# Performance work log

Hardware: AMD Instinct MI355X
Metric: run time of the kernel (lower is better)

Reference implementation:

```python
import jax, jax.numpy as jnp
import numpy as np

HID = 2048
HEADS = 16
HEAD = HID // HEADS  # 128
INTER = 8192
EPS = 1e-5
THETA = 10000.0
B, S = 2, 2048


def _layernorm(x, scale, bias):
    mu = jnp.mean(x, axis=-1, keepdims=True)
    var = jnp.var(x, axis=-1, keepdims=True)
    return (x - mu) * jax.lax.rsqrt(var + EPS) * scale + bias


def _rope(x, cos, sin):
    # x: [b,s,h,d]; adjacent pairs form complex numbers (per apply_rotary_emb)
    xr = x.reshape(*x.shape[:-1], HEAD // 2, 2)
    x0, x1 = xr[..., 0], xr[..., 1]
    o0 = x0 * cos - x1 * sin
    o1 = x0 * sin + x1 * cos
    return jnp.stack((o0, o1), axis=-1).reshape(x.shape)


def setup_inputs() -> dict:
    key = jax.random.key(0)
    ks = jax.random.split(key, 6)
    sc = 0.02
    return {
        "hidden_states": jax.random.normal(ks[0], (B, S, HID), jnp.float32),
        "attention_mask": jnp.zeros((B, 1, 1, S), jnp.float32),
        "w_qkv": (jax.random.normal(ks[1], (HID, 3 * HID), jnp.float32) * sc),
        "b_qkv": jnp.zeros((3 * HID,), jnp.float32),
        "w_o": (jax.random.normal(ks[2], (HID, HID), jnp.float32) * sc),
        "b_o": jnp.zeros((HID,), jnp.float32),
        "ln1_scale": jnp.ones((HID,), jnp.float32),
        "ln1_bias": jnp.zeros((HID,), jnp.float32),
        "ln2_scale": jnp.ones((HID,), jnp.float32),
        "ln2_bias": jnp.zeros((HID,), jnp.float32),
        "w_in": (jax.random.normal(ks[3], (HID, INTER), jnp.float32) * sc),
        "b_in": jnp.zeros((INTER,), jnp.float32),
        "w_out": (jax.random.normal(ks[4], (INTER, HID), jnp.float32) * sc),
        "b_out": jnp.zeros((HID,), jnp.float32),
    }


def reference(hidden_states, attention_mask, w_qkv, b_qkv, w_o, b_o,
              ln1_scale, ln1_bias, ln2_scale, ln2_bias,
              w_in, b_in, w_out, b_out):
    b, s, d = hidden_states.shape
    # ---- attention branch ----
    x1 = _layernorm(hidden_states, ln1_scale, ln1_bias)
    qkv = x1 @ w_qkv + b_qkv
    q, k, v = jnp.split(qkv, 3, axis=-1)
    q = q.reshape(b, s, HEADS, HEAD)
    k = k.reshape(b, s, HEADS, HEAD)
    v = v.reshape(b, s, HEADS, HEAD)
    # rotary embedding (complex pairing of adjacent elements)
    inv_freq = 1.0 / (THETA ** (jnp.arange(0, HEAD, 2, dtype=jnp.float32) / HEAD))
    freqs = jnp.arange(s, dtype=jnp.float32)[:, None] * inv_freq[None, :]  # [s, HEAD/2]
    cos = jnp.cos(freqs)[None, :, None, :]
    sin = jnp.sin(freqs)[None, :, None, :]
    q = _rope(q, cos, sin)
    k = _rope(k, cos, sin)
    # NOTE: source multiplies by sqrt(head_size) (faithful to original code)
    factor = jnp.sqrt(jnp.float32(HEAD))
    attn = jnp.einsum('bqhd,bkhd->bhqk', q, k) * factor  # [b,h,s,s]
    causal = jnp.tril(jnp.ones((s, s), dtype=bool))
    bias = jnp.where(causal, 0.0, jnp.finfo(jnp.float32).min)
    attn = attn + bias[None, None, :, :] + attention_mask
    p = jax.nn.softmax(attn, axis=-1)
    ao = jnp.einsum('bhqk,bkhd->bqhd', p, v).reshape(b, s, d)
    attn_out = ao @ w_o + b_o
    # ---- mlp branch (parallel residual) ----
    x2 = _layernorm(hidden_states, ln2_scale, ln2_bias)
    mlp = jax.nn.gelu(x2 @ w_in + b_in, approximate=False) @ w_out + b_out
    return mlp + hidden_states + attn_out
```

## Files before the change

### kernel.cpp

```cpp
#include <hip/hip_runtime.h>
#include <math.h>

#define HID 2048
#define NH 16
#define HD 128
#define INTER 8192
#define BB 2
#define SS 2048
#define MT (BB*SS)

typedef __bf16 bf16x8 __attribute__((ext_vector_type(8)));
typedef _Float16 f16x8 __attribute__((ext_vector_type(8)));
typedef float f32x4 __attribute__((ext_vector_type(4)));
typedef float f32x16 __attribute__((ext_vector_type(16)));
typedef unsigned short u16x8 __attribute__((ext_vector_type(8)));

__device__ __forceinline__ float bf2f(unsigned short u) {
  unsigned v = ((unsigned)u) << 16;
  return __builtin_bit_cast(float, v);
}
__device__ __forceinline__ unsigned short f2bf(float x) {
  unsigned u = __builtin_bit_cast(unsigned, x);
  u += 0x7fffu + ((u >> 16) & 1u);
  return (unsigned short)(u >> 16);
}
__device__ __forceinline__ unsigned short f2h(float x) {
  _Float16 h = (_Float16)x;
  return __builtin_bit_cast(unsigned short, h);
}
__device__ __forceinline__ void gll16(const void* g, const void* lds) {
  __builtin_amdgcn_global_load_lds(
      (const __attribute__((address_space(1))) void*)g,
      (__attribute__((address_space(3))) void*)lds, 16, 0, 0);
}
__device__ __forceinline__ int swz(int row) {
  return (row & 7) ^ ((row >> 2) & 4);
}

__global__ __launch_bounds__(256) void ln2k(
    const float* __restrict__ X, const float* __restrict__ s1,
    const float* __restrict__ b1, const float* __restrict__ s2,
    const float* __restrict__ b2, unsigned short* __restrict__ X1f,
    unsigned short* __restrict__ X2) {
  const int row = blockIdx.x;
  const int tid = threadIdx.x;
  const float* x = X + (long)row * HID;
  float4 v0 = ((const float4*)x)[tid * 2];
  float4 v1 = ((const float4*)x)[tid * 2 + 1];
  float s = v0.x + v0.y + v0.z + v0.w + v1.x + v1.y + v1.z + v1.w;
  float q = v0.x * v0.x + v0.y * v0.y + v0.z * v0.z + v0.w * v0.w +
            v1.x * v1.x + v1.y * v1.y + v1.z * v1.z + v1.w * v1.w;
#pragma unroll
  for (int off = 1; off < 64; off <<= 1) {
    s += __shfl_xor(s, off);
    q += __shfl_xor(q, off);
  }
  __shared__ float rs[4], rq[4];
  const int wid = tid >> 6, lane = tid & 63;
  if (lane == 0) { rs[wid] = s; rq[wid] = q; }
  __syncthreads();
  s = rs[0] + rs[1] + rs[2] + rs[3];
  q = rq[0] + rq[1] + rq[2] + rq[3];
  const float mu = s * (1.f / HID);
  const float var = q * (1.f / HID) - mu * mu;
  const float rstd = rsqrtf(var + 1e-5f);
  float xv[8] = {v0.x, v0.y, v0.z, v0.w, v1.x, v1.y, v1.z, v1.w};
  u16x8 o1, o2;
#pragma unroll
  for (int e = 0; e < 8; e++) {
    const int j = tid * 8 + e;
    const float xn = (xv[e] - mu) * rstd;
    o1[e] = f2h(xn * s1[j] + b1[j]);
    o2[e] = f2bf(xn * s2[j] + b2[j]);
  }
  *(u16x8*)(X1f + (long)row * HID + tid * 8) = o1;
  *(u16x8*)(X2 + (long)row * HID + tid * 8) = o2;
}

template <bool F16>
__global__ __launch_bounds__(256) void wtrans(const float* __restrict__ W,
                                              unsigned short* __restrict__ WT,
                                              int K, int N, int ldn, int coff) {
  (void)N;
  __shared__ float t[32][33];
  const int n0 = blockIdx.x * 32, k0 = blockIdx.y * 32;
  const int tx = threadIdx.x, ty = threadIdx.y;
#pragma unroll
  for (int r = 0; r < 4; r++)
    t[ty + r * 8][tx] = W[(long)(k0 + ty + r * 8) * ldn + coff + n0 + tx];
  __syncthreads();
#pragma unroll
  for (int r = 0; r < 4; r++) {
    const float v = t[tx][ty + r * 8];
    WT[(long)(n0 + ty + r * 8) * K + k0 + tx] = F16 ? f2h(v) : f2bf(v);
  }
}

__global__ void rope_tab(float2* __restrict__ rope) {
  const int s = blockIdx.x, i = threadIdx.x;
  const double ang = (double)s * pow(10000.0, -(double)i / 64.0);
  rope[s * 64 + i] = make_float2((float)cos(ang), (float)sin(ang));
}

__global__ __launch_bounds__(256) void gemmqkv(
    const unsigned short* __restrict__ A, const unsigned short* __restrict__ Bt,
    const float* __restrict__ bias, const float2* __restrict__ rope,
    unsigned short* __restrict__ QF, unsigned short* __restrict__ KF,
    unsigned short* __restrict__ Vb) {
  __shared__ unsigned short As[128 * 64];
  __shared__ unsigned short Bs[128 * 64];
  const int K = HID;
  const int tid = threadIdx.x;
  const int wid = tid >> 6, lane = tid & 63;
  const int l31 = lane & 31, lg = lane >> 5;
  const int wr = wid >> 1, wc = wid & 1;
  const long rA0 = (long)blockIdx.y * 128;
  const long rB0 = (long)blockIdx.x * 128;

  f32x16 acc[2][2] = {};

  for (int kt = 0; kt < K; kt += 64) {
#pragma unroll
    for (int i = 0; i < 4; i++) {
      const int lin = i * 4096 + wid * 1024 + (lane << 4);
      const int row = lin >> 7;
      const int cs = ((lin >> 4) & 7) ^ swz(row);
      gll16(A + (rA0 + row) * (long)K + kt + cs * 8,
            (const char*)As + (i * 4096 + wid * 1024));
      gll16(Bt + (rB0 + row) * (long)K + kt + cs * 8,
            (const char*)Bs + (i * 4096 + wid * 1024));
    }
    __syncthreads();
#pragma unroll
    for (int kk = 0; kk < 4; kk++) {
      f16x8 av[2], bv[2];
#pragma unroll
      for (int t = 0; t < 2; t++) {
        const int rowA = wr * 64 + t * 32 + l31;
        const int cha = (kk * 2 + lg) ^ swz(rowA);
        av[t] = *(const f16x8*)((const char*)As + rowA * 128 + cha * 16);
        const int rowB = wc * 64 + t * 32 + l31;
        const int chb = (kk * 2 + lg) ^ swz(rowB);
        bv[t] = *(const f16x8*)((const char*)Bs + rowB * 128 + chb * 16);
      }
#pragma unroll
      for (int mt = 0; mt < 2; mt++)
#pragma unroll
        for (int nt = 0; nt < 2; nt++)
          acc[mt][nt] = __builtin_amdgcn_mfma_f32_32x32x16_f16(
              av[mt], bv[nt], acc[mt][nt], 0, 0, 0);
    }
    __syncthreads();
  }

  const int b_ = (int)(rA0 >> 11);
#pragma unroll
  for (int mt = 0; mt < 2; mt++) {
#pragma unroll
    for (int nt = 0; nt < 2; nt++) {
      const int col = (int)rB0 + wc * 64 + nt * 32 + l31;
      const float bsv = bias[col];
      const int cq = col & 2047;
      const int i = (cq & 127) >> 1;
      const int hh = (cq >> 7) & 15;
      const int d = cq & 127;
#pragma unroll
      for (int reg = 0; reg < 16; reg++) {
        const int row = (int)rA0 + wr * 64 + mt * 32 + (reg & 3) +
                        8 * (reg >> 2) + 4 * lg;
        const int srow = row & 2047;
        const float v = acc[mt][nt][reg] + bsv;
        if (col < 4096) {
          const float p = __shfl_xor(v, 1);
          const float2 cs = rope[srow * 64 + i];
          const float o = ((lane & 1) == 0) ? (v * cs.x - p * cs.y)
                                            : (p * cs.y + v * cs.x);
          unsigned short* dst = (col < 2048) ? QF : KF;
          dst[((long)(b_ * NH + hh) * SS + srow) * HD + d] = f2h(o);
        } else {
          Vb[(long)row * HID + (col - 4096)] = f2bf(v);
        }
      }
    }
  }
}

__global__ __launch_bounds__(256) void vtrans(
    const unsigned short* __restrict__ Vb, unsigned short* __restrict__ VTb) {
  __shared__ unsigned short t[32][33];
  const int bh = blockIdx.z, b = bh >> 4, h = bh & 15;
  const int d0 = blockIdx.x * 32, s0 = blockIdx.y * 32;
  const int tx = threadIdx.x, ty = threadIdx.y;
#pragma unroll
  for (int r = 0; r < 4; r++) {
    const int s = s0 + ty + r * 8;
    t[ty + r * 8][tx] = Vb[((long)(b * SS + s)) * HID + h * HD + d0 + tx];
  }
  __syncthreads();
#pragma unroll
  for (int r = 0; r < 4; r++) {
    const int d = d0 + ty + r * 8;
    VTb[((long)bh * HD + d) * SS + s0 + tx] = t[tx][ty + r * 8];
  }
}

template <int MODE>
__global__ __launch_bounds__(256) void gemm128(
    const unsigned short* __restrict__ A, const unsigned short* __restrict__ Bt,
    const float* __restrict__ bias, void* __restrict__ Cout, int M, int N,
    int K, const float* __restrict__ residF,
    const unsigned short* __restrict__ residB) {
  (void)M;
  __shared__ unsigned short As[128 * 64];
  __shared__ unsigned short Bs[128 * 64];
  const int tid = threadIdx.x;
  const int wid = tid >> 6, lane = tid & 63;
  const int l31 = lane & 31, lg = lane >> 5;
  const int wr = wid >> 1, wc = wid & 1;
  const long rA0 = (long)blockIdx.y * 128;
  const long rB0 = (long)blockIdx.x * 128;

  f32x16 acc[2][2] = {};

  for (int kt = 0; kt < K; kt += 64) {
#pragma unroll
    for (int i = 0; i < 4; i++) {
      const int lin = i * 4096 + wid * 1024 + (lane << 4);
      const int row = lin >> 7;
      const int cs = ((lin >> 4) & 7) ^ swz(row);
      gll16(A + (rA0 + row) * (long)K + kt + cs * 8,
            (const char*)As + (i * 4096 + wid * 1024));
      gll16(Bt + (rB0 + row) * (long)K + kt + cs * 8,
            (const char*)Bs + (i * 4096 + wid * 1024));
    }
    __syncthreads();
#pragma unroll
    for (int kk = 0; kk < 4; kk++) {
      bf16x8 av[2], bv[2];
#pragma unroll
      for (int t = 0; t < 2; t++) {
        const int rowA = wr * 64 + t * 32 + l31;
        const int cha = (kk * 2 + lg) ^ swz(rowA);
        av[t] = *(const bf16x8*)((const char*)As + rowA * 128 + cha * 16);
        const int rowB = wc * 64 + t * 32 + l31;
        const int chb = (kk * 2 + lg) ^ swz(rowB);
        bv[t] = *(const bf16x8*)((const char*)Bs + rowB * 128 + chb * 16);
      }
#pragma unroll
      for (int mt = 0; mt < 2; mt++)
#pragma unroll
        for (int nt = 0; nt < 2; nt++)
          acc[mt][nt] = __builtin_amdgcn_mfma_f32_32x32x16_bf16(
              av[mt], bv[nt], acc[mt][nt], 0, 0, 0);
    }
    __syncthreads();
  }

#pragma unroll
  for (int mt = 0; mt < 2; mt++) {
#pragma unroll
    for (int nt = 0; nt < 2; nt++) {
      const long col = rB0 + wc * 64 + nt * 32 + l31;
      const float bsv = bias[col];
#pragma unroll
      for (int reg = 0; reg < 16; reg++) {
        const long row = rA0 + wr * 64 + mt * 32 + (reg & 3) +
                         8 * (reg >> 2) + 4 * lg;
        float v = acc[mt][nt][reg] + bsv;
        if (MODE == 1) v = 0.5f * v * (1.f + erff(v * 0.7071067811865475f));
        if (MODE == 2) {
          v += residF[row * N + col] + bf2f(residB[row * N + col]);
          ((float*)Cout)[row * N + col] = v;
        } else {
          ((unsigned short*)Cout)[row * N + col] = f2bf(v);
        }
      }
    }
  }
}

__global__ __launch_bounds__(512, 2) void flash(
    const unsigned short* __restrict__ QF, const unsigned short* __restrict__ KF,
    const unsigned short* __restrict__ VT, const float* __restrict__ amask,
    unsigned short* __restrict__ AO) {
  __shared__ unsigned short Kt[2][64 * 128];
  __shared__ unsigned short Vt[2][128 * 64];
  __shared__ unsigned short Pl[8 * 1024];
  __shared__ float maskL[SS];
  const int z = blockIdx.x;
  const int qt = 15 - (z >> 5);
  const int bh = z & 31;
  const int b = bh >> 4, h = bh & 15;
  const int tid = threadIdx.x, wid = tid >> 6, lane = tid & 63;
  const int l16 = lane & 15, lhi = lane >> 4;
  const unsigned short* Qfb = QF + (long)bh * SS * HD;
  const unsigned short* Kfb = KF + (long)bh * SS * HD;
  const unsigned short* Vb = VT + (long)bh * HD * SS;
  const int q0 = qt * 128 + wid * 16;
  const float LOG2E = 1.4426950408889634f;
  const float SCL2 = 16.322232154552f;

  {
    float4 m0 = ((const float4*)(amask + (long)b * SS))[tid];
    m0.x *= LOG2E; m0.y *= LOG2E; m0.z *= LOG2E; m0.w *= LOG2E;
    ((float4*)maskL)[tid] = m0;
  }

  f16x8 qf[4];
#pragma unroll
  for (int ks = 0; ks < 4; ks++)
    qf[ks] = *(const f16x8*)(Qfb + (long)(q0 + l16) * HD + ks * 32 + lhi * 8);

  auto stage = [&](int kt2, int bu) {
#pragma unroll
    for (int i = 0; i < 2; i++) {
      const int lin = i * 8192 + wid * 1024 + (lane << 4);
      const int dst = i * 8192 + wid * 1024;
      {
        const int row = lin >> 8;
        const int cs = ((lin >> 4) & 15) ^ (row & 7);
        gll16(Kfb + (long)(kt2 * 64 + row) * HD + cs * 8,
              (const char*)Kt[bu] + dst);
      }
      {
        const int row = lin >> 7;
        const int cs = ((lin >> 4) & 7) ^ (row & 7);
        gll16(Vb + (long)row * SS + kt2 * 64 + cs * 8, (const char*)Vt[bu] + dst);
      }
    }
  };

  f32x4 accO[8] = {};
  float mrow[4], lrow[4];
#pragma unroll
  for (int r = 0; r < 4; r++) { mrow[r] = -3e38f; lrow[r] = 0.f; }

  const int nkt = 2 * qt + 2;
  stage(0, 0);
  asm volatile("s_waitcnt lgkmcnt(0)" ::: "memory");
  int buf = 0;
  for (int kt = 0; kt < nkt; kt++) {
    if (kt + 1 < nkt) {
      stage(kt + 1, buf ^ 1);
      asm volatile("s_waitcnt vmcnt(4)" ::: "memory");
    } else {
      asm volatile("s_waitcnt vmcnt(0)" ::: "memory");
    }
    __builtin_amdgcn_s_barrier();

    const bool active = (kt * 64 <= q0 + 15);
    if (active) {
      f32x4 accS[4] = {};
      __builtin_amdgcn_s_setprio(1);
#pragma unroll
      for (int ks = 0; ks < 4; ks++) {
        f16x8 bk[4];
#pragma unroll
        for (int nf = 0; nf < 4; nf++) {
          const int row = nf * 16 + l16;
          const int ch = (ks * 4 + lhi) ^ (row & 7);
          bk[nf] = *(const f16x8*)((const char*)Kt[buf] + row * 256 + ch * 16);
        }
#pragma unroll
        for (int nf = 0; nf < 4; nf++)
          accS[nf] = __builtin_amdgcn_mfma_f32_16x16x32_f16(qf[ks], bk[nf],
                                                            accS[nf], 0, 0, 0);
      }
      __builtin_amdgcn_s_setprio(0);

      float mk[4];
#pragma unroll
      for (int nf = 0; nf < 4; nf++) mk[nf] = maskL[kt * 64 + nf * 16 + l16];
#pragma unroll
      for (int nf = 0; nf < 4; nf++)
#pragma unroll
        for (int r = 0; r < 4; r++) {
          const int key = kt * 64 + nf * 16 + l16;
          const int qg = q0 + lhi * 4 + r;
          const float sv = accS[nf][r] * SCL2 + mk[nf];
          accS[nf][r] = (key > qg) ? -1e30f : sv;
        }

      float mx[4];
#pragma unroll
      for (int r = 0; r < 4; r++) {
        float m0 = fmaxf(fmaxf(accS[0][r], accS[1][r]),
                         fmaxf(accS[2][r], accS[3][r]));
        m0 = fmaxf(m0, __shfl_xor(m0, 1));
        m0 = fmaxf(m0, __shfl_xor(m0, 2));
        m0 = fmaxf(m0, __shfl_xor(m0, 4));
        m0 = fmaxf(m0, __shfl_xor(m0, 8));
        mx[r] = m0;
      }
      bool defer = true;
#pragma unroll
      for (int r = 0; r < 4; r++) defer = defer && (mx[r] <= mrow[r] + 8.f);
      if (!__all(defer)) {
#pragma unroll
        for (int r = 0; r < 4; r++) {
          const float mnew = fmaxf(mrow[r], mx[r]);
          const float alpha = exp2f(mrow[r] - mnew);
          mrow[r] = mnew;
          lrow[r] *= alpha;
#pragma unroll
          for (int nf2 = 0; nf2 < 8; nf2++) accO[nf2][r] *= alpha;
        }
      }
#pragma unroll
      for (int r = 0; r < 4; r++) {
        const int rowl = lhi * 4 + r;
        const int qg = q0 + rowl;
        float rsum = 0.f;
#pragma unroll
        for (int nf = 0; nf < 4; nf++) {
          const int key = kt * 64 + nf * 16 + l16;
          const float p = (key > qg) ? 0.f : exp2f(accS[nf][r] - mrow[r]);
          rsum += p;
          const int colv = nf * 16 + l16;
          const int slot = (colv >> 3) ^ (rowl & 7);
          *(unsigned short*)((char*)Pl + wid * 2048 + rowl * 128 + slot * 16 +
                             (colv & 7) * 2) = f2bf(p);
        }
        rsum += __shfl_xor(rsum, 1);
        rsum += __shfl_xor(rsum, 2);
        rsum += __shfl_xor(rsum, 4);
        rsum += __shfl_xor(rsum, 8);
        lrow[r] += rsum;
      }

      __builtin_amdgcn_s_setprio(1);
#pragma unroll
      for (int ks2 = 0; ks2 < 2; ks2++) {
        const int chp = (ks2 * 4 + lhi) ^ (l16 & 7);
        bf16x8 pa =
            *(const bf16x8*)((const char*)Pl + wid * 2048 + l16 * 128 + chp * 16);
#pragma unroll
        for (int nf2 = 0; nf2 < 8; nf2++) {
          const int rowv = nf2 * 16 + l16;
          const int ch = (ks2 * 4 + lhi) ^ (rowv & 7);
          bf16x8 vv =
              *(const bf16x8*)((const char*)Vt[buf] + rowv * 128 + ch * 16);
          accO[nf2] = __builtin_amdgcn_mfma_f32_16x16x32_bf16(pa, vv,
                                                              accO[nf2], 0, 0, 0);
        }
      }
      __builtin_amdgcn_s_setprio(0);
    }
    __builtin_amdgcn_s_barrier();
    buf ^= 1;
  }

#pragma unroll
  for (int nf2 = 0; nf2 < 8; nf2++)
#pragma unroll
    for (int r = 0; r < 4; r++) {
      const int qg = q0 + lhi * 4 + r;
      const int d = nf2 * 16 + l16;
      const float v = accO[nf2][r] / lrow[r];
      AO[((long)(b * SS + qg)) * HID + h * HD + d] = f2bf(v);
    }
}

extern "C" void kernel_launch(void* const* d_in, const int* in_sizes, int n_in,
                              void* d_out, int out_size, void* d_ws,
                              size_t ws_size, hipStream_t stream) {
  (void)in_sizes; (void)n_in; (void)out_size;
  const float* hidden = (const float*)d_in[0];
  const float* amask = (const float*)d_in[1];
  const float* w_qkv = (const float*)d_in[2];
  const float* b_qkv = (const float*)d_in[3];
  const float* w_o = (const float*)d_in[4];
  const float* b_o = (const float*)d_in[5];
  const float* ln1s = (const float*)d_in[6];
  const float* ln1b = (const float*)d_in[7];
  const float* ln2s = (const float*)d_in[8];
  const float* ln2b = (const float*)d_in[9];
  const float* w_in = (const float*)d_in[10];
  const float* b_in = (const float*)d_in[11];
  const float* w_out = (const float*)d_in[12];
  const float* b_out = (const float*)d_in[13];

  char* ws = (char*)d_ws;
  unsigned short* X1f = (unsigned short*)(ws + 0);
  unsigned short* X2  = (unsigned short*)(ws + 16777216);
  unsigned short* Vbf = (unsigned short*)(ws + 33554432);
  unsigned short* WQ  = (unsigned short*)(ws + 50331648);
  unsigned short* QFb = (unsigned short*)(ws + 75497472);
  unsigned short* KFb = (unsigned short*)(ws + 92274688);
  unsigned short* VTb = (unsigned short*)(ws + 109051904);
  unsigned short* ATT = (unsigned short*)(ws + 125829120);
  unsigned short* WD  = (unsigned short*)(ws + 142606336);
  float2* ROPE = (float2*)(ws + 176160768);
  if (ws_size < 177209344) return;

  unsigned short* AO = X1f;
  unsigned short* H1 = WQ;

  ln2k<<<MT, 256, 0, stream>>>(hidden, ln1s, ln1b, ln2s, ln2b, X1f, X2);
  rope_tab<<<SS, 64, 0, stream>>>(ROPE);
  wtrans<true><<<dim3(192, 64), dim3(32, 8), 0, stream>>>(w_qkv, WQ, HID,
                                                          3 * HID, 3 * HID, 0);
  gemmqkv<<<dim3(48, 32), 256, 0, stream>>>(X1f, WQ, b_qkv, ROPE, QFb, KFb,
                                            Vbf);
  vtrans<<<dim3(4, 64, 32), dim3(32, 8), 0, stream>>>(Vbf, VTb);
  flash<<<512, 512, 0, stream>>>(QFb, KFb, VTb, amask, AO);
  wtrans<false><<<dim3(64, 64), dim3(32, 8), 0, stream>>>(w_o, WD, HID, HID,
                                                          HID, 0);
  gemm128<0><<<dim3(16, 32), 256, 0, stream>>>(AO, WD, b_o, ATT, MT, HID, HID,
                                               nullptr, nullptr);
  wtrans<false><<<dim3(256, 64), dim3(32, 8), 0, stream>>>(w_in, WD, HID,
                                                           INTER, INTER, 0);
  gemm128<1><<<dim3(64, 32), 256, 0, stream>>>(X2, WD, b_in, H1, MT, INTER,
                                               HID, nullptr, nullptr);
  wtrans<false><<<dim3(64, 256), dim3(32, 8), 0, stream>>>(w_out, WD, INTER,
                                                           HID, HID, 0);
  gemm128<2><<<dim3(16, 32), 256, 0, stream>>>(H1, WD, b_out, d_out, MT, HID,
                                               INTER, hidden, ATT);
}
```

Baseline: 757.8 us.

## Double-buffer GEMM LDS tiles with async prefetch and XCD-aware block remap

Both the QKV GEMM and the generic 128x128 GEMM now use two LDS buffers. The next K-tile is loaded with global-to-LDS loads while the current tile feeds MFMAs, using vmcnt waits instead of full syncthreads. Block indices are remapped so neighbouring tiles land on the same XCD for better L2 reuse, and s_setprio raises priority around MFMA bursts. The cost is twice the LDS per block, which may lower occupancy, and the hand-written waitcnt and barrier ordering must stay correct.

Result: slower. 818.3 us (+8.0%).

```diff
diff --git a/kernel.cpp b/kernel.cpp
--- a/kernel.cpp
+++ b/kernel.cpp
@@ -102,35 +102,56 @@
   rope[s * 64 + i] = make_float2((float)cos(ang), (float)sin(ang));
 }
 
+__device__ __forceinline__ int2 xcd_map() {
+  const int nwg = gridDim.x * gridDim.y;
+  const int flat = blockIdx.y * gridDim.x + blockIdx.x;
+  const int w2 = (flat & 7) * (nwg >> 3) + (flat >> 3);
+  return make_int2(w2 % gridDim.x, w2 / gridDim.x);
+}
+
 __global__ __launch_bounds__(256) void gemmqkv(
     const unsigned short* __restrict__ A, const unsigned short* __restrict__ Bt,
     const float* __restrict__ bias, const float2* __restrict__ rope,
     unsigned short* __restrict__ QF, unsigned short* __restrict__ KF,
     unsigned short* __restrict__ Vb) {
-  __shared__ unsigned short As[128 * 64];
-  __shared__ unsigned short Bs[128 * 64];
+  __shared__ unsigned short As[2][128 * 64];
+  __shared__ unsigned short Bs[2][128 * 64];
   const int K = HID;
   const int tid = threadIdx.x;
   const int wid = tid >> 6, lane = tid & 63;
   const int l31 = lane & 31, lg = lane >> 5;
   const int wr = wid >> 1, wc = wid & 1;
-  const long rA0 = (long)blockIdx.y * 128;
-  const long rB0 = (long)blockIdx.x * 128;
+  const int2 bb = xcd_map();
+  const long rA0 = (long)bb.y * 128;
+  const long rB0 = (long)bb.x * 128;
 
   f32x16 acc[2][2] = {};
 
-  for (int kt = 0; kt < K; kt += 64) {
+  auto stage = [&](int kt2, int bu) {
 #pragma unroll
     for (int i = 0; i < 4; i++) {
       const int lin = i * 4096 + wid * 1024 + (lane << 4);
       const int row = lin >> 7;
       const int cs = ((lin >> 4) & 7) ^ swz(row);
-      gll16(A + (rA0 + row) * (long)K + kt + cs * 8,
-            (const char*)As + (i * 4096 + wid * 1024));
-      gll16(Bt + (rB0 + row) * (long)K + kt + cs * 8,
-            (const char*)Bs + (i * 4096 + wid * 1024));
-    }
-    __syncthreads();
+      const int dst = i * 4096 + wid * 1024;
+      gll16(A + (rA0 + row) * (long)K + kt2 * 64 + cs * 8,
+            (const char*)As[bu] + dst);
+      gll16(Bt + (rB0 + row) * (long)K + kt2 * 64 + cs * 8,
+            (const char*)Bs[bu] + dst);
+    }
+  };
+
+  const int nkt = K / 64;
+  stage(0, 0);
+  int buf = 0;
+  for (int kt = 0; kt < nkt; kt++) {
+    if (kt + 1 < nkt) {
+      stage(kt + 1, buf ^ 1);
+      asm volatile("s_waitcnt vmcnt(8)" ::: "memory");
+    } else {
+      asm volatile("s_waitcnt vmcnt(0)" ::: "memory");
+    }
+    __builtin_amdgcn_s_barrier();
 #pragma unroll
     for (int kk = 0; kk < 4; kk++) {
       f16x8 av[2], bv[2];
@@ -138,19 +159,22 @@
       for (int t = 0; t < 2; t++) {
         const int rowA = wr * 64 + t * 32 + l31;
         const int cha = (kk * 2 + lg) ^ swz(rowA);
-        av[t] = *(const f16x8*)((const char*)As + rowA * 128 + cha * 16);
+        av[t] = *(const f16x8*)((const char*)As[buf] + rowA * 128 + cha * 16);
         const int rowB = wc * 64 + t * 32 + l31;
         const int chb = (kk * 2 + lg) ^ swz(rowB);
-        bv[t] = *(const f16x8*)((const char*)Bs + rowB * 128 + chb * 16);
-      }
+        bv[t] = *(const f16x8*)((const char*)Bs[buf] + rowB * 128 + chb * 16);
+      }
+      __builtin_amdgcn_s_setprio(1);
 #pragma unroll
       for (int mt = 0; mt < 2; mt++)
 #pragma unroll
         for (int nt = 0; nt < 2; nt++)
           acc[mt][nt] = __builtin_amdgcn_mfma_f32_32x32x16_f16(
               av[mt], bv[nt], acc[mt][nt], 0, 0, 0);
-    }
-    __syncthreads();
+      __builtin_amdgcn_s_setprio(0);
+    }
+    __builtin_amdgcn_s_barrier();
+    buf ^= 1;
   }
 
   const int b_ = (int)(rA0 >> 11);
@@ -211,29 +235,43 @@
     int K, const float* __restrict__ residF,
     const unsigned short* __restrict__ residB) {
   (void)M;
-  __shared__ unsigned short As[128 * 64];
-  __shared__ unsigned short Bs[128 * 64];
+  __shared__ unsigned short As[2][128 * 64];
+  __shared__ unsigned short Bs[2][128 * 64];
   const int tid = threadIdx.x;
   const int wid = tid >> 6, lane = tid & 63;
   const int l31 = lane & 31, lg = lane >> 5;
   const int wr = wid >> 1, wc = wid & 1;
-  const long rA0 = (long)blockIdx.y * 128;
-  const long rB0 = (long)blockIdx.x * 128;
+  const int2 bb = xcd_map();
+  const long rA0 = (long)bb.y * 128;
+  const long rB0 = (long)bb.x * 128;
 
   f32x16 acc[2][2] = {};
 
-  for (int kt = 0; kt < K; kt += 64) {
+  auto stage = [&](int kt2, int bu) {
 #pragma unroll
     for (int i = 0; i < 4; i++) {
       const int lin = i * 4096 + wid * 1024 + (lane << 4);
       const int row = lin >> 7;
       const int cs = ((lin >> 4) & 7) ^ swz(row);
-      gll16(A + (rA0 + row) * (long)K + kt + cs * 8,
-            (const char*)As + (i * 4096 + wid * 1024));
-      gll16(Bt + (rB0 + row) * (long)K + kt + cs * 8,
-            (const char*)Bs + (i * 4096 + wid * 1024));
-    }
-    __syncthreads();
+      const int dst = i * 4096 + wid * 1024;
+      gll16(A + (rA0 + row) * (long)K + kt2 * 64 + cs * 8,
+            (const char*)As[bu] + dst);
+      gll16(Bt + (rB0 + row) * (long)K + kt2 * 64 + cs * 8,
+            (const char*)Bs[bu] + dst);
+    }
+  };
+
+  const int nkt = K / 64;
+  stage(0, 0);
+  int buf = 0;
+  for (int kt = 0; kt < nkt; kt++) {
+    if (kt + 1 < nkt) {
+      stage(kt + 1, buf ^ 1);
+      asm volatile("s_waitcnt vmcnt(8)" ::: "memory");
+    } else {
+      asm volatile("s_waitcnt vmcnt(0)" ::: "memory");
+    }
+    __builtin_amdgcn_s_barrier();
 #pragma unroll
     for (int kk = 0; kk < 4; kk++) {
       bf16x8 av[2], bv[2];
@@ -241,19 +279,22 @@
       for (int t = 0; t < 2; t++) {
         const int rowA = wr * 64 + t * 32 + l31;
         const int cha = (kk * 2 + lg) ^ swz(rowA);
-        av[t] = *(const bf16x8*)((const char*)As + rowA * 128 + cha * 16);
+        av[t] = *(const bf16x8*)((const char*)As[buf] + rowA * 128 + cha * 16);
         const int rowB = wc * 64 + t * 32 + l31;
         const int chb = (kk * 2 + lg) ^ swz(rowB);
-        bv[t] = *(const bf16x8*)((const char*)Bs + rowB * 128 + chb * 16);
-      }
+        bv[t] = *(const bf16x8*)((const char*)Bs[buf] + rowB * 128 + chb * 16);
+      }
+      __builtin_amdgcn_s_setprio(1);
 #pragma unroll
       for (int mt = 0; mt < 2; mt++)
 #pragma unroll
         for (int nt = 0; nt < 2; nt++)
           acc[mt][nt] = __builtin_amdgcn_mfma_f32_32x32x16_bf16(
               av[mt], bv[nt], acc[mt][nt], 0, 0, 0);
-    }
-    __syncthreads();
+      __builtin_amdgcn_s_setprio(0);
+    }
+    __builtin_amdgcn_s_barrier();
+    buf ^= 1;
   }
 
 #pragma unroll
```
